# Kernel optimization log

Measured on AMD Instinct MI355X. Metric: run time of the kernel, lower is better.

Reference implementation:

```python
import jax, jax.numpy as jnp
import numpy as np

N_HEAD = 8
N_FEAT = 512
D_K = N_FEAT // N_HEAD


def setup_inputs() -> dict:
    key0 = jax.random.key(0)
    ks = jax.random.split(key0, 12)
    B, C, T, S = 16, 6, 512, 8
    scale = 1.0 / np.sqrt(N_FEAT)
    inp = {
        "query": jax.random.normal(ks[0], (B, C, T, N_FEAT), jnp.float32),
        "key": jax.random.normal(ks[1], (B, S, N_FEAT), jnp.float32),
        "value": jax.random.normal(ks[2], (B, S, N_FEAT), jnp.float32),
        "mask": jnp.ones((B, 1, T, S), jnp.int32),
        "Wq": jax.random.normal(ks[3], (N_FEAT, N_FEAT), jnp.float32) * scale,
        "bq": jax.random.normal(ks[4], (N_FEAT,), jnp.float32) * scale,
        "Wk": jax.random.normal(ks[5], (N_FEAT, N_FEAT), jnp.float32) * scale,
        "bk": jax.random.normal(ks[6], (N_FEAT,), jnp.float32) * scale,
        "Wv": jax.random.normal(ks[7], (N_FEAT, N_FEAT), jnp.float32) * scale,
        "bv": jax.random.normal(ks[8], (N_FEAT,), jnp.float32) * scale,
        "Wo": jax.random.normal(ks[9], (N_FEAT, N_FEAT), jnp.float32) * scale,
        "bo": jax.random.normal(ks[10], (N_FEAT,), jnp.float32) * scale,
    }
    return inp


def reference(query, key, value, mask, Wq, bq, Wk, bk, Wv, bv, Wo, bo):
    B, C, T, F = query.shape
    S = key.shape[-2]
    h, d_k = N_HEAD, D_K
    inv_sqrt_dk = 1.0 / jnp.sqrt(jnp.asarray(d_k, query.dtype))

    # forward_qkv
    qx = jnp.swapaxes(query, 1, 2)                       # (B, T, C, F)
    q = (qx @ Wq.T + bq).reshape(B, T, C, h, d_k)        # (B, T, C, h, d_k)
    k = (key @ Wk.T + bk).reshape(B, S, h, d_k)          # (B, S, h, d_k)
    v = (value @ Wv.T + bv).reshape(B, S, h, d_k)        # (B, S, h, d_k)
    v2 = jnp.swapaxes(q, 2, 3)                           # (B, T, h, C, d_k)
    q1 = q.mean(axis=2)                                  # (B, T, h, d_k)

    # stage 1: mean-pooled query attends over spk_num (masked softmax)
    scores = jnp.einsum('bthd,bshd->bhts', q1, k) * inv_sqrt_dk  # (B, h, T, S)
    m = (mask == 0)                                      # (B, 1, T, S) bool
    scores = jnp.where(m, -jnp.inf, scores)
    attn = jax.nn.softmax(scores, axis=-1)
    attn = jnp.where(m, 0.0, attn)
    phone_ctx = jnp.einsum('bhts,bshd->bthd', attn, v)   # (B, T, h, d_k)

    # stage 2: pooled context attends over channels
    ss = jnp.einsum('bthd,bthcd->bthc', phone_ctx, v2) * inv_sqrt_dk  # (B, T, h, C)
    attn2 = jax.nn.softmax(ss, axis=-1)
    x = jnp.einsum('bthc,bthcd->bthd', attn2, v2).reshape(B, T, h * d_k)
    return x @ Wo.T + bo                                 # (B, T, F)
```

## Files before the change

### kernel.cpp

```cpp
#include <hip/hip_runtime.h>
#include <hip/hip_bf16.h>

#define B_  16
#define C_  6
#define T_  512
#define S_  8

#define AS1 __attribute__((address_space(1)))
#define AS3 __attribute__((address_space(3)))

typedef __attribute__((ext_vector_type(8))) short bf16x8;
typedef __attribute__((ext_vector_type(4))) float f32x4;

__device__ __forceinline__ ushort f2bf(float f) {
    __hip_bfloat16 h = __float2bfloat16(f);
    return *reinterpret_cast<ushort*>(&h);
}
__device__ __forceinline__ float bfu2f(ushort u) {
    uint x = (uint)u << 16;
    union { uint u; float f; } c; c.u = x; return c.f;
}

__global__ void convert_all(const float* __restrict__ Wq, const float* __restrict__ Wo,
                            const float* __restrict__ Wk, const float* __restrict__ Wv,
                            const float* __restrict__ key, const float* __restrict__ value,
                            ushort* __restrict__ dWq, ushort* __restrict__ dWo,
                            ushort* __restrict__ dWk, ushort* __restrict__ dWv,
                            ushort* __restrict__ dkey, ushort* __restrict__ dval) {
    int y = blockIdx.y;
    int i = (blockIdx.x * 256 + threadIdx.x) * 4;
    if (y < 4) {
        const float* s = (y == 0) ? Wq : (y == 1) ? Wo : (y == 2) ? Wk : Wv;
        ushort* d = (y == 0) ? dWq : (y == 1) ? dWo : (y == 2) ? dWk : dWv;
        float4 v = *(const float4*)(s + i);
        ushort4 o;
        o.x = f2bf(v.x); o.y = f2bf(v.y); o.z = f2bf(v.z); o.w = f2bf(v.w);
        *(ushort4*)(d + i) = o;
    } else if (i < 65536) {
        float4 v = *(const float4*)(key + i);
        ushort4 o;
        o.x = f2bf(v.x); o.y = f2bf(v.y); o.z = f2bf(v.z); o.w = f2bf(v.w);
        *(ushort4*)(dkey + i) = o;
        float4 v2 = *(const float4*)(value + i);
        ushort4 o2;
        o2.x = f2bf(v2.x); o2.y = f2bf(v2.y); o2.z = f2bf(v2.z); o2.w = f2bf(v2.w);
        *(ushort4*)(dval + i) = o2;
    }
}

__global__ __launch_bounds__(256, 2) void kvgemm(const ushort* __restrict__ keybf,
                                                 const ushort* __restrict__ valbf,
                                                 const ushort* __restrict__ Wkbf,
                                                 const ushort* __restrict__ Wvbf,
                                                 const float* __restrict__ bk,
                                                 const float* __restrict__ bv,
                                                 float* __restrict__ kout,
                                                 float* __restrict__ vout) {
    __shared__ __align__(16) ushort lds[32768];

    const int kv = blockIdx.x >> 2;
    const int bn = (blockIdx.x & 3) * 128;
    const ushort* Ain = kv ? valbf : keybf;
    const ushort* Wbf = kv ? Wvbf : Wkbf;
    const float* bias = kv ? bv : bk;
    float* out = kv ? vout : kout;

    const int tid  = threadIdx.x;
    const int lane = tid & 63;
    const int wv   = tid >> 6;
    const int wm   = (wv >> 1) * 64;
    const int wn   = (wv & 1) * 64;
    const int ln15 = lane & 15;
    const int ln16 = lane >> 4;

    auto GLDS = [&](const ushort* gbase, int rowbase, ushort* ldsbase, int k0) {
        int rb = wv * 32 + (lane >> 3);
        int c  = lane & 7;
#pragma unroll
        for (int i = 0; i < 4; ++i) {
            int r = rb + i * 8;
            const ushort* src = gbase + (long)(rowbase + r) * 512 + k0 + ((c ^ (r & 7)) << 3);
            ushort* dst = ldsbase + wv * 2048 + i * 512;
            __builtin_amdgcn_global_load_lds((AS1 const void*)src, (AS3 void*)dst, 16, 0, 0);
        }
    };

    ushort* asb0 = lds;
    ushort* asb1 = lds + 8192;
    ushort* wsb[2] = { lds + 16384, lds + 24576 };

    f32x4 acc[4][4] = {};

    auto MFMA_PHASE = [&](ushort* Asb, ushort* Wsb) {
        __builtin_amdgcn_s_setprio(1);
#pragma unroll
        for (int kj = 0; kj < 2; ++kj) {
            bf16x8 af[4], bfv[4];
#pragma unroll
            for (int mi = 0; mi < 4; ++mi) {
                int row = wm + mi * 16 + ln15;
                int ch  = kj * 4 + ln16;
                af[mi] = *(const bf16x8*)&Asb[row * 64 + ((ch ^ (row & 7)) << 3)];
            }
#pragma unroll
            for (int ni = 0; ni < 4; ++ni) {
                int row = wn + ni * 16 + ln15;
                int ch  = kj * 4 + ln16;
                bfv[ni] = *(const bf16x8*)&Wsb[row * 64 + ((ch ^ (row & 7)) << 3)];
            }
#pragma unroll
            for (int mi = 0; mi < 4; ++mi)
#pragma unroll
                for (int ni = 0; ni < 4; ++ni)
                    acc[mi][ni] = __builtin_amdgcn_mfma_f32_16x16x32_bf16(
                        af[mi], bfv[ni], acc[mi][ni], 0, 0, 0);
        }
        __builtin_amdgcn_s_setprio(0);
    };

    GLDS(Ain, 0, asb0, 0);
    GLDS(Wbf, bn, wsb[0], 0);
    asm volatile("s_waitcnt vmcnt(0) lgkmcnt(0)" ::: "memory");
    __builtin_amdgcn_sched_barrier(0);
    __builtin_amdgcn_s_barrier();
    asm volatile("" ::: "memory");
#pragma unroll
    for (int kt = 0; kt < 8; ++kt) {
        ushort* Asb = (kt & 1) ? asb1 : asb0;
        ushort* nAs = (kt & 1) ? asb0 : asb1;
        if (kt < 7) {
            GLDS(Wbf, bn, wsb[(kt + 1) & 1], (kt + 1) * 64);
            GLDS(Ain, 0, nAs, (kt + 1) * 64);
        }
        __builtin_amdgcn_sched_barrier(0);
        MFMA_PHASE(Asb, wsb[kt & 1]);
        asm volatile("s_waitcnt vmcnt(0) lgkmcnt(0)" ::: "memory");
        __builtin_amdgcn_sched_barrier(0);
        __builtin_amdgcn_s_barrier();
        asm volatile("" ::: "memory");
    }

    float bsv[4];
#pragma unroll
    for (int ni = 0; ni < 4; ++ni)
        bsv[ni] = bias[bn + wn + ni * 16 + ln15];

    float* ef = (float*)lds;
#pragma unroll
    for (int half = 0; half < 2; ++half) {
        if (wm == half * 64) {
#pragma unroll
            for (int mi = 0; mi < 4; ++mi)
#pragma unroll
                for (int j = 0; j < 4; ++j) {
                    int lr = mi * 16 + ln16 * 4 + j;
#pragma unroll
                    for (int ni = 0; ni < 4; ++ni) {
                        int col = wn + ni * 16 + ln15;
                        int cs  = col ^ ((lr & 12) << 2);
                        ef[lr * 128 + cs] = acc[mi][ni][j] + bsv[ni];
                    }
                }
        }
        asm volatile("s_waitcnt lgkmcnt(0)" ::: "memory");
        __builtin_amdgcn_sched_barrier(0);
        __builtin_amdgcn_s_barrier();
        asm volatile("" ::: "memory");
#pragma unroll
        for (int i = 0; i < 8; ++i) {
            int idx = i * 1024 + tid * 4;
            int lr = idx >> 7, col = idx & 127;
            int cs = col ^ ((lr & 12) << 2);
            float4 v = *(const float4*)&ef[lr * 128 + cs];
            *(float4*)(out + (long)(half * 64 + lr) * 512 + bn + col) = v;
        }
        if (half == 0) {
            asm volatile("" ::: "memory");
            __builtin_amdgcn_s_barrier();
            asm volatile("" ::: "memory");
        }
    }
}

__global__ __launch_bounds__(512) void qattn(const float* __restrict__ query,
                                             const ushort* __restrict__ Wqbf,
                                             const float* __restrict__ bq,
                                             const float* __restrict__ kproj,
                                             const float* __restrict__ vproj,
                                             const int* __restrict__ mask,
                                             ushort* __restrict__ xout) {
    __shared__ __align__(16) ushort Abf[2][96 * 128];
    __shared__ __align__(16) ushort xstage[16 * 512];
    __shared__ int mlds[256];

    const int b   = blockIdx.x >> 4;
    const int tpb = (blockIdx.x & 15) << 5;
    const int tid = threadIdx.x;
    const int h    = tid >> 6;
    const int lane = tid & 63;
    const int ln15 = lane & 15;
    const int ln16 = lane >> 4;
    const int nb   = h * 64;

    float4 ra[6];
    f32x4 acc[6][4];
    uint4 br[3][4];

    auto LOADQ = [&](int t0, int q) {
#pragma unroll
        for (int i = 0; i < 6; ++i) {
            int idx = i * 2048 + tid * 4;
            int row = idx >> 7;
            int col = idx & 127;
            int c = row >> 4, tt = row & 15;
            ra[i] = *(const float4*)(query + ((long)(b * 6 + c) * 512 + t0 + tt) * 512
                                     + q * 128 + col);
        }
    };
    auto WRITEQ = [&](ushort* buf) {
#pragma unroll
        for (int i = 0; i < 6; ++i) {
            int idx = i * 2048 + tid * 4;
            int row = idx >> 7;
            int col = idx & 127;
            int kc8  = col >> 3;
            int half = (col >> 2) & 1;
            int s = (kc8 & 8) | ((kc8 & 7) ^ (row & 7));
            ushort4 p;
            p.x = f2bf(ra[i].x); p.y = f2bf(ra[i].y);
            p.z = f2bf(ra[i].z); p.w = f2bf(ra[i].w);
            *(ushort4*)((char*)buf + row * 256 + s * 16 + half * 8) = p;
        }
    };
    auto RINGINIT = [&]() {
#pragma unroll
        for (int kb = 0; kb < 3; ++kb)
#pragma unroll
            for (int nf = 0; nf < 4; ++nf)
                br[kb][nf] = *(const uint4*)(Wqbf + (long)(nb + nf * 16 + ln15) * 512
                                             + kb * 32 + ln16 * 8);
    };
#define GEMMQ(BUF, Q)                                                          \
    {                                                                          \
        const ushort* buf_ = (BUF);                                            \
        __builtin_amdgcn_s_setprio(1);                                         \
        _Pragma("unroll")                                                      \
        for (int kb8 = 0; kb8 < 4; ++kb8) {                                    \
            int kb = (Q) * 4 + kb8;                                            \
            bf16x8 af[6];                                                      \
            _Pragma("unroll")                                                  \
            for (int mf = 0; mf < 6; ++mf) {                                   \
                int row = mf * 16 + ln15;                                      \
                int kc8 = kb8 * 4 + ln16;                                      \
                int s = (kc8 & 8) | ((kc8 & 7) ^ (row & 7));                   \
                af[mf] = *(const bf16x8*)((const char*)buf_ + row * 256 + s * 16); \
            }                                                                  \
            _Pragma("unroll")                                                  \
            for (int mf = 0; mf < 6; ++mf)                                     \
                _Pragma("unroll")                                              \
                for (int nf = 0; nf < 4; ++nf)                                 \
                    acc[mf][nf] = __builtin_amdgcn_mfma_f32_16x16x32_bf16(     \
                        af[mf], *(const bf16x8*)&br[kb % 3][nf], acc[mf][nf], 0, 0, 0); \
            if (kb < 13) {                                                     \
                _Pragma("unroll")                                              \
                for (int nf = 0; nf < 4; ++nf)                                 \
                    br[(kb + 3) % 3][nf] = *(const uint4*)(Wqbf +              \
                        (long)(nb + nf * 16 + ln15) * 512 + (kb + 3) * 32 + ln16 * 8); \
            }                                                                  \
        }                                                                      \
        __builtin_amdgcn_s_setprio(0);                                         \
    }

    auto PHASES = [&](int t0, int mloff) {
        {
            float bqv[4];
#pragma unroll
            for (int nf = 0; nf < 4; ++nf) bqv[nf] = bq[nb + nf * 16 + ln15];
#pragma unroll
            for (int mf = 0; mf < 6; ++mf)
#pragma unroll
                for (int nf = 0; nf < 4; ++nf)
#pragma unroll
                    for (int j = 0; j < 4; ++j) acc[mf][nf][j] += bqv[nf];
        }
        f32x4 q1f[4];
#pragma unroll
        for (int nf = 0; nf < 4; ++nf) {
            f32x4 s = acc[0][nf];
#pragma unroll
            for (int c = 1; c < 6; ++c) s += acc[c][nf];
            q1f[nf] = s * (1.0f / 6.0f);
        }
        float sc[4][8];
#pragma unroll
        for (int s = 0; s < 8; ++s) {
            float kv[4];
#pragma unroll
            for (int nf = 0; nf < 4; ++nf)
                kv[nf] = kproj[(long)(b * 8 + s) * 512 + nb + nf * 16 + ln15];
#pragma unroll
            for (int j = 0; j < 4; ++j) {
                float p = q1f[0][j] * kv[0] + q1f[1][j] * kv[1]
                        + q1f[2][j] * kv[2] + q1f[3][j] * kv[3];
                p += __shfl_xor(p, 1); p += __shfl_xor(p, 2);
                p += __shfl_xor(p, 4); p += __shfl_xor(p, 8);
                sc[j][s] = p * 0.125f;
            }
        }
#pragma unroll
        for (int j = 0; j < 4; ++j) {
            int tt = ln16 * 4 + j;
            int mk[8];
            float mx = -1e30f;
#pragma unroll
            for (int s = 0; s < 8; ++s) {
                mk[s] = mlds[mloff + tt * 8 + s];
                if (mk[s] == 0) sc[j][s] = -1e30f;
                mx = fmaxf(mx, sc[j][s]);
            }
            float sum = 0.f;
#pragma unroll
            for (int s = 0; s < 8; ++s) {
                float e = __expf(sc[j][s] - mx);
                sc[j][s] = e;
                sum += e;
            }
            float inv = 1.0f / sum;
#pragma unroll
            for (int s = 0; s < 8; ++s) sc[j][s] = mk[s] ? sc[j][s] * inv : 0.f;
        }
        f32x4 pcf[4] = {};
#pragma unroll
        for (int s = 0; s < 8; ++s) {
            float vv[4];
#pragma unroll
            for (int nf = 0; nf < 4; ++nf)
                vv[nf] = vproj[(long)(b * 8 + s) * 512 + nb + nf * 16 + ln15];
#pragma unroll
            for (int nf = 0; nf < 4; ++nf)
#pragma unroll
                for (int j = 0; j < 4; ++j) pcf[nf][j] += sc[j][s] * vv[nf];
        }
        float a2[4][6];
#pragma unroll
        for (int c = 0; c < 6; ++c)
#pragma unroll
            for (int j = 0; j < 4; ++j) {
                float p = pcf[0][j] * acc[c][0][j] + pcf[1][j] * acc[c][1][j]
                        + pcf[2][j] * acc[c][2][j] + pcf[3][j] * acc[c][3][j];
                p += __shfl_xor(p, 1); p += __shfl_xor(p, 2);
                p += __shfl_xor(p, 4); p += __shfl_xor(p, 8);
                a2[j][c] = p * 0.125f;
            }
#pragma unroll
        for (int j = 0; j < 4; ++j) {
            float mx = -1e30f;
#pragma unroll
            for (int c = 0; c < 6; ++c) mx = fmaxf(mx, a2[j][c]);
            float sum = 0.f;
#pragma unroll
            for (int c = 0; c < 6; ++c) {
                float e = __expf(a2[j][c] - mx);
                a2[j][c] = e;
                sum += e;
            }
            float inv = 1.0f / sum;
#pragma unroll
            for (int c = 0; c < 6; ++c) a2[j][c] *= inv;
        }
#pragma unroll
        for (int nf = 0; nf < 4; ++nf)
#pragma unroll
            for (int j = 0; j < 4; ++j) {
                float x = 0.f;
#pragma unroll
                for (int c = 0; c < 6; ++c) x += a2[j][c] * acc[c][nf][j];
                xstage[(ln16 * 4 + j) * 512 + nb + nf * 16 + ln15] = f2bf(x);
            }
        __syncthreads();
        {
            int idx = tid * 16;
            int row = idx >> 9;
            int off = idx & 511;
            uint4 v0 = *(const uint4*)&xstage[row * 512 + off];
            uint4 v1 = *(const uint4*)&xstage[row * 512 + off + 8];
            ushort* dst = xout + ((long)(b * 512 + t0 + row)) * 512 + off;
            *(uint4*)dst = v0;
            *(uint4*)(dst + 8) = v1;
        }
    };

    const int t0a = tpb;
    const int t0b = tpb + 16;

    if (tid < 256) mlds[tid] = mask[((long)b * 512 + tpb + (tid >> 3)) * 8 + (tid & 7)];

    LOADQ(t0a, 0);
    WRITEQ(Abf[0]);
    __syncthreads();

#pragma unroll
    for (int mf = 0; mf < 6; ++mf)
#pragma unroll
        for (int nf = 0; nf < 4; ++nf) acc[mf][nf] = (f32x4){0.f, 0.f, 0.f, 0.f};
    RINGINIT();

    LOADQ(t0a, 1); __builtin_amdgcn_sched_barrier(0);
    GEMMQ(Abf[0], 0);
    WRITEQ(Abf[1]); __syncthreads();
    LOADQ(t0a, 2); __builtin_amdgcn_sched_barrier(0);
    GEMMQ(Abf[1], 1);
    WRITEQ(Abf[0]); __syncthreads();
    LOADQ(t0a, 3); __builtin_amdgcn_sched_barrier(0);
    GEMMQ(Abf[0], 2);
    WRITEQ(Abf[1]); __syncthreads();
    LOADQ(t0b, 0); __builtin_amdgcn_sched_barrier(0);
    GEMMQ(Abf[1], 3);
    WRITEQ(Abf[0]); __syncthreads();

    LOADQ(t0b, 1); __builtin_amdgcn_sched_barrier(0);
    PHASES(t0a, 0);

    __syncthreads();
    WRITEQ(Abf[1]);
    __syncthreads();

#pragma unroll
    for (int mf = 0; mf < 6; ++mf)
#pragma unroll
        for (int nf = 0; nf < 4; ++nf) acc[mf][nf] = (f32x4){0.f, 0.f, 0.f, 0.f};
    RINGINIT();

    LOADQ(t0b, 2); __builtin_amdgcn_sched_barrier(0);
    GEMMQ(Abf[0], 0);
    WRITEQ(Abf[0]); __syncthreads();
    LOADQ(t0b, 3); __builtin_amdgcn_sched_barrier(0);
    GEMMQ(Abf[1], 1);
    WRITEQ(Abf[1]); __syncthreads();
    GEMMQ(Abf[0], 2);
    __syncthreads();
    GEMMQ(Abf[1], 3);

    PHASES(t0b, 128);
#undef GEMMQ
}

__global__ __launch_bounds__(256, 2)
void gemm_mfma(const void* __restrict__ Ain,
               const ushort* __restrict__ Wbf,
               const float* __restrict__ bias,
               void* __restrict__ out, int mpanels) {
    __shared__ __align__(16) ushort lds[32768];

    const int bid = blockIdx.x;
    const int cpx = (mpanels * 4) >> 3;
    const int swz = (bid & 7) * cpx + (bid >> 3);
    const int bm = (swz >> 2) * 128;
    const int bn = (swz & 3) * 128;

    const int tid  = threadIdx.x;
    const int lane = tid & 63;
    const int wv   = tid >> 6;
    const int wm   = (wv >> 1) * 64;
    const int wn   = (wv & 1) * 64;
    const int ln15 = lane & 15;
    const int ln16 = lane >> 4;

    auto GLDS = [&](const ushort* gbase, int rowbase, ushort* ldsbase, int k0) {
        int rb = wv * 32 + (lane >> 3);
        int c  = lane & 7;
#pragma unroll
        for (int i = 0; i < 4; ++i) {
            int r = rb + i * 8;
            const ushort* src = gbase + (long)(rowbase + r) * 512 + k0 + ((c ^ (r & 7)) << 3);
            ushort* dst = ldsbase + wv * 2048 + i * 512;
            __builtin_amdgcn_global_load_lds((AS1 const void*)src, (AS3 void*)dst, 16, 0, 0);
        }
    };

    ushort* asb0 = lds;
    ushort* asb1 = lds + 8192;
    ushort* wsb[2] = { lds + 16384, lds + 24576 };

    f32x4 acc[4][4] = {};

    auto MFMA_PHASE = [&](ushort* Asb, ushort* Wsb) {
        __builtin_amdgcn_s_setprio(1);
#pragma unroll
        for (int kj = 0; kj < 2; ++kj) {
            bf16x8 af[4], bfv[4];
#pragma unroll
            for (int mi = 0; mi < 4; ++mi) {
                int row = wm + mi * 16 + ln15;
                int ch  = kj * 4 + ln16;
                af[mi] = *(const bf16x8*)&Asb[row * 64 + ((ch ^ (row & 7)) << 3)];
            }
#pragma unroll
            for (int ni = 0; ni < 4; ++ni) {
                int row = wn + ni * 16 + ln15;
                int ch  = kj * 4 + ln16;
                bfv[ni] = *(const bf16x8*)&Wsb[row * 64 + ((ch ^ (row & 7)) << 3)];
            }
#pragma unroll
            for (int mi = 0; mi < 4; ++mi)
#pragma unroll
                for (int ni = 0; ni < 4; ++ni)
                    acc[mi][ni] = __builtin_amdgcn_mfma_f32_16x16x32_bf16(
                        af[mi], bfv[ni], acc[mi][ni], 0, 0, 0);
        }
        __builtin_amdgcn_s_setprio(0);
    };

    GLDS((const ushort*)Ain, bm, asb0, 0);
    GLDS(Wbf, bn, wsb[0], 0);
    asm volatile("s_waitcnt vmcnt(0) lgkmcnt(0)" ::: "memory");
    __builtin_amdgcn_sched_barrier(0);
    __builtin_amdgcn_s_barrier();
    asm volatile("" ::: "memory");
#pragma unroll
    for (int kt = 0; kt < 8; ++kt) {
        ushort* Asb = (kt & 1) ? asb1 : asb0;
        ushort* nAs = (kt & 1) ? asb0 : asb1;
        if (kt < 7) {
            GLDS(Wbf, bn, wsb[(kt + 1) & 1], (kt + 1) * 64);
            GLDS((const ushort*)Ain, bm, nAs, (kt + 1) * 64);
        }
        __builtin_amdgcn_sched_barrier(0);
        MFMA_PHASE(Asb, wsb[kt & 1]);
        asm volatile("s_waitcnt vmcnt(0) lgkmcnt(0)" ::: "memory");
        __builtin_amdgcn_sched_barrier(0);
        __builtin_amdgcn_s_barrier();
        asm volatile("" ::: "memory");
    }

    float bsv[4];
#pragma unroll
    for (int ni = 0; ni < 4; ++ni)
        bsv[ni] = bias[bn + wn + ni * 16 + ln15];

    float* ef = (float*)lds;
#pragma unroll
    for (int half = 0; half < 2; ++half) {
        if (wm == half * 64) {
#pragma unroll
            for (int mi = 0; mi < 4; ++mi)
#pragma unroll
                for (int j = 0; j < 4; ++j) {
                    int lr = mi * 16 + ln16 * 4 + j;
#pragma unroll
                    for (int ni = 0; ni < 4; ++ni) {
                        int col = wn + ni * 16 + ln15;
                        int cs  = col ^ ((lr & 12) << 2);
                        ef[lr * 128 + cs] = acc[mi][ni][j] + bsv[ni];
                    }
                }
        }
        asm volatile("s_waitcnt lgkmcnt(0)" ::: "memory");
        __builtin_amdgcn_sched_barrier(0);
        __builtin_amdgcn_s_barrier();
        asm volatile("" ::: "memory");
#pragma unroll
        for (int i = 0; i < 8; ++i) {
            int idx = i * 1024 + tid * 4;
            int lr = idx >> 7, col = idx & 127;
            int cs = col ^ ((lr & 12) << 2);
            float4 v = *(const float4*)&ef[lr * 128 + cs];
            *(float4*)((float*)out + (long)(bm + half * 64 + lr) * 512 + bn + col) = v;
        }
        if (half == 0) {
            asm volatile("" ::: "memory");
            __builtin_amdgcn_s_barrier();
            asm volatile("" ::: "memory");
        }
    }
}

extern "C" void kernel_launch(void* const* d_in, const int* in_sizes, int n_in,
                              void* d_out, int out_size, void* d_ws, size_t ws_size,
                              hipStream_t stream) {
    const float* query = (const float*)d_in[0];
    const float* key   = (const float*)d_in[1];
    const float* value = (const float*)d_in[2];
    const int*   mask  = (const int*)d_in[3];
    const float* Wq = (const float*)d_in[4];
    const float* bq = (const float*)d_in[5];
    const float* Wk = (const float*)d_in[6];
    const float* bk = (const float*)d_in[7];
    const float* Wv = (const float*)d_in[8];
    const float* bv = (const float*)d_in[9];
    const float* Wo = (const float*)d_in[10];
    const float* bo = (const float*)d_in[11];
    float* out = (float*)d_out;

    char* ws = (char*)d_ws;
    ushort* Wqbf  = (ushort*)(ws + 0);
    ushort* Wobf  = (ushort*)(ws + 524288u);
    ushort* Wkbf  = (ushort*)(ws + 1048576u);
    ushort* Wvbf  = (ushort*)(ws + 1572864u);
    ushort* keybf = (ushort*)(ws + 2097152u);
    ushort* valbf = (ushort*)(ws + 2228224u);
    float*  kproj = (float*)(ws + 2621440u);
    float*  vproj = (float*)(ws + 2883584u);
    ushort* xbf   = (ushort*)(ws + (4u << 20));

    convert_all<<<dim3(256, 5), 256, 0, stream>>>(Wq, Wo, Wk, Wv, key, value,
                                                  Wqbf, Wobf, Wkbf, Wvbf, keybf, valbf);

    kvgemm<<<8, 256, 0, stream>>>(keybf, valbf, Wkbf, Wvbf, bk, bv, kproj, vproj);

    qattn<<<256, 512, 0, stream>>>(query, Wqbf, bq, kproj, vproj, mask, xbf);

    gemm_mfma<<<256, 256, 0, stream>>>(xbf, Wobf, bo, out, 64);

    (void)in_sizes; (void)n_in; (void)out_size; (void)ws_size;
}
```

Measured before the change: 95.08 us.

## Split qattn into one 16-timestep tile per block with two blocks per CU

The qattn kernel now processes a single 16-timestep tile per block instead of two sequential tiles, launching 512 blocks instead of 256. It requests two 512-thread blocks per CU via launch bounds, reuses the A buffer as the output staging area to cut LDS, and uses two register sets to prefetch query chunks. The aim is more concurrency, so one block's GEMM overlaps another's softmax/epilogue and load latency, instead of serial in-block pipelining. The tighter register budget may cause spills, and the Wq fragments are reloaded per block.

New measurement: 83.48 us, median of 2. -12.2%, faster.

```diff
diff --git a/kernel.cpp b/kernel.cpp
--- a/kernel.cpp
+++ b/kernel.cpp
@@ -182,19 +182,18 @@
     }
 }
 
-__global__ __launch_bounds__(512) void qattn(const float* __restrict__ query,
-                                             const ushort* __restrict__ Wqbf,
-                                             const float* __restrict__ bq,
-                                             const float* __restrict__ kproj,
-                                             const float* __restrict__ vproj,
-                                             const int* __restrict__ mask,
-                                             ushort* __restrict__ xout) {
+__global__ __launch_bounds__(512, 2) void qattn(const float* __restrict__ query,
+                                                const ushort* __restrict__ Wqbf,
+                                                const float* __restrict__ bq,
+                                                const float* __restrict__ kproj,
+                                                const float* __restrict__ vproj,
+                                                const int* __restrict__ mask,
+                                                ushort* __restrict__ xout) {
     __shared__ __align__(16) ushort Abf[2][96 * 128];
-    __shared__ __align__(16) ushort xstage[16 * 512];
-    __shared__ int mlds[256];
-
-    const int b   = blockIdx.x >> 4;
-    const int tpb = (blockIdx.x & 15) << 5;
+    __shared__ int mlds[128];
+
+    const int b   = blockIdx.x >> 5;
+    const int t0  = (blockIdx.x & 31) << 4;
     const int tid = threadIdx.x;
     const int h    = tid >> 6;
     const int lane = tid & 63;
@@ -202,11 +201,9 @@
     const int ln16 = lane >> 4;
     const int nb   = h * 64;
 
-    float4 ra[6];
-    f32x4 acc[6][4];
-    uint4 br[3][4];
-
-    auto LOADQ = [&](int t0, int q) {
+    float4 ra0[6], ra1[6];
+
+    auto LOADQ = [&](float4 (&ra)[6], int q) {
 #pragma unroll
         for (int i = 0; i < 6; ++i) {
             int idx = i * 2048 + tid * 4;
@@ -217,7 +214,7 @@
                                      + q * 128 + col);
         }
     };
-    auto WRITEQ = [&](ushort* buf) {
+    auto WRITEQ = [&](float4 (&ra)[6], ushort* buf) {
 #pragma unroll
         for (int i = 0; i < 6; ++i) {
             int idx = i * 2048 + tid * 4;
@@ -232,14 +229,24 @@
             *(ushort4*)((char*)buf + row * 256 + s * 16 + half * 8) = p;
         }
     };
-    auto RINGINIT = [&]() {
-#pragma unroll
-        for (int kb = 0; kb < 3; ++kb)
-#pragma unroll
-            for (int nf = 0; nf < 4; ++nf)
-                br[kb][nf] = *(const uint4*)(Wqbf + (long)(nb + nf * 16 + ln15) * 512
-                                             + kb * 32 + ln16 * 8);
-    };
+
+    if (tid < 128) mlds[tid] = mask[((long)b * 512 + t0 + (tid >> 3)) * 8 + (tid & 7)];
+
+    LOADQ(ra0, 0);
+    WRITEQ(ra0, Abf[0]);
+    LOADQ(ra1, 1);
+    __builtin_amdgcn_sched_barrier(0);
+    __syncthreads();
+
+    f32x4 acc[6][4] = {};
+    uint4 br[3][4];
+#pragma unroll
+    for (int kb = 0; kb < 3; ++kb)
+#pragma unroll
+        for (int nf = 0; nf < 4; ++nf)
+            br[kb][nf] = *(const uint4*)(Wqbf + (long)(nb + nf * 16 + ln15) * 512
+                                         + kb * 32 + ln16 * 8);
+
 #define GEMMQ(BUF, Q)                                                          \
     {                                                                          \
         const ushort* buf_ = (BUF);                                            \
@@ -271,178 +278,146 @@
         __builtin_amdgcn_s_setprio(0);                                         \
     }
 
-    auto PHASES = [&](int t0, int mloff) {
-        {
-            float bqv[4];
-#pragma unroll
-            for (int nf = 0; nf < 4; ++nf) bqv[nf] = bq[nb + nf * 16 + ln15];
-#pragma unroll
-            for (int mf = 0; mf < 6; ++mf)
-#pragma unroll
-                for (int nf = 0; nf < 4; ++nf)
-#pragma unroll
-                    for (int j = 0; j < 4; ++j) acc[mf][nf][j] += bqv[nf];
-        }
-        f32x4 q1f[4];
-#pragma unroll
-        for (int nf = 0; nf < 4; ++nf) {
-            f32x4 s = acc[0][nf];
-#pragma unroll
-            for (int c = 1; c < 6; ++c) s += acc[c][nf];
-            q1f[nf] = s * (1.0f / 6.0f);
-        }
-        float sc[4][8];
+    LOADQ(ra0, 2);
+    __builtin_amdgcn_sched_barrier(0);
+    GEMMQ(Abf[0], 0);
+    WRITEQ(ra1, Abf[1]);
+    __syncthreads();
+
+    LOADQ(ra1, 3);
+    __builtin_amdgcn_sched_barrier(0);
+    GEMMQ(Abf[1], 1);
+    WRITEQ(ra0, Abf[0]);
+    __syncthreads();
+
+    GEMMQ(Abf[0], 2);
+    WRITEQ(ra1, Abf[1]);
+    __syncthreads();
+
+    GEMMQ(Abf[1], 3);
+#undef GEMMQ
+
+    {
+        float bqv[4];
+#pragma unroll
+        for (int nf = 0; nf < 4; ++nf) bqv[nf] = bq[nb + nf * 16 + ln15];
+#pragma unroll
+        for (int mf = 0; mf < 6; ++mf)
+#pragma unroll
+            for (int nf = 0; nf < 4; ++nf)
+#pragma unroll
+                for (int j = 0; j < 4; ++j) acc[mf][nf][j] += bqv[nf];
+    }
+
+    f32x4 q1f[4];
+#pragma unroll
+    for (int nf = 0; nf < 4; ++nf) {
+        f32x4 s = acc[0][nf];
+#pragma unroll
+        for (int c = 1; c < 6; ++c) s += acc[c][nf];
+        q1f[nf] = s * (1.0f / 6.0f);
+    }
+
+    float sc[4][8];
+#pragma unroll
+    for (int s = 0; s < 8; ++s) {
+        float kv[4];
+#pragma unroll
+        for (int nf = 0; nf < 4; ++nf)
+            kv[nf] = kproj[(long)(b * 8 + s) * 512 + nb + nf * 16 + ln15];
+#pragma unroll
+        for (int j = 0; j < 4; ++j) {
+            float p = q1f[0][j] * kv[0] + q1f[1][j] * kv[1]
+                    + q1f[2][j] * kv[2] + q1f[3][j] * kv[3];
+            p += __shfl_xor(p, 1); p += __shfl_xor(p, 2);
+            p += __shfl_xor(p, 4); p += __shfl_xor(p, 8);
+            sc[j][s] = p * 0.125f;
+        }
+    }
+#pragma unroll
+    for (int j = 0; j < 4; ++j) {
+        int tt = ln16 * 4 + j;
+        int mk[8];
+        float mx = -1e30f;
 #pragma unroll
         for (int s = 0; s < 8; ++s) {
-            float kv[4];
-#pragma unroll
-            for (int nf = 0; nf < 4; ++nf)
-                kv[nf] = kproj[(long)(b * 8 + s) * 512 + nb + nf * 16 + ln15];
-#pragma unroll
-            for (int j = 0; j < 4; ++j) {
-                float p = q1f[0][j] * kv[0] + q1f[1][j] * kv[1]
-                        + q1f[2][j] * kv[2] + q1f[3][j] * kv[3];
-                p += __shfl_xor(p, 1); p += __shfl_xor(p, 2);
-                p += __shfl_xor(p, 4); p += __shfl_xor(p, 8);
-                sc[j][s] = p * 0.125f;
-            }
-        }
+            mk[s] = mlds[tt * 8 + s];
+            if (mk[s] == 0) sc[j][s] = -1e30f;
+            mx = fmaxf(mx, sc[j][s]);
+        }
+        float sum = 0.f;
+#pragma unroll
+        for (int s = 0; s < 8; ++s) {
+            float e = __expf(sc[j][s] - mx);
+            sc[j][s] = e;
+            sum += e;
+        }
+        float inv = 1.0f / sum;
+#pragma unroll
+        for (int s = 0; s < 8; ++s) sc[j][s] = mk[s] ? sc[j][s] * inv : 0.f;
+    }
+    f32x4 pcf[4] = {};
+#pragma unroll
+    for (int s = 0; s < 8; ++s) {
+        float vv[4];
+#pragma unroll
+        for (int nf = 0; nf < 4; ++nf)
+            vv[nf] = vproj[(long)(b * 8 + s) * 512 + nb + nf * 16 + ln15];
+#pragma unroll
+        for (int nf = 0; nf < 4; ++nf)
+#pragma unroll
+            for (int j = 0; j < 4; ++j) pcf[nf][j] += sc[j][s] * vv[nf];
+    }
+
+    float a2[4][6];
+#pragma unroll
+    for (int c = 0; c < 6; ++c)
 #pragma unroll
         for (int j = 0; j < 4; ++j) {
-            int tt = ln16 * 4 + j;
-            int mk[8];
-            float mx = -1e30f;
-#pragma unroll
-            for (int s = 0; s < 8; ++s) {
-                mk[s] = mlds[mloff + tt * 8 + s];
-                if (mk[s] == 0) sc[j][s] = -1e30f;
-                mx = fmaxf(mx, sc[j][s]);
-            }
-            float sum = 0.f;
-#pragma unroll
-            for (int s = 0; s < 8; ++s) {
-                float e = __expf(sc[j][s] - mx);
-                sc[j][s] = e;
-                sum += e;
-            }
-            float inv = 1.0f / sum;
-#pragma unroll
-            for (int s = 0; s < 8; ++s) sc[j][s] = mk[s] ? sc[j][s] * inv : 0.f;
-        }
-        f32x4 pcf[4] = {};
-#pragma unroll
-        for (int s = 0; s < 8; ++s) {
-            float vv[4];
-#pragma unroll
-            for (int nf = 0; nf < 4; ++nf)
-                vv[nf] = vproj[(long)(b * 8 + s) * 512 + nb + nf * 16 + ln15];
-#pragma unroll
-            for (int nf = 0; nf < 4; ++nf)
-#pragma unroll
-                for (int j = 0; j < 4; ++j) pcf[nf][j] += sc[j][s] * vv[nf];
-        }
-        float a2[4][6];
-#pragma unroll
-        for (int c = 0; c < 6; ++c)
-#pragma unroll
-            for (int j = 0; j < 4; ++j) {
-                float p = pcf[0][j] * acc[c][0][j] + pcf[1][j] * acc[c][1][j]
-                        + pcf[2][j] * acc[c][2][j] + pcf[3][j] * acc[c][3][j];
-                p += __shfl_xor(p, 1); p += __shfl_xor(p, 2);
-                p += __shfl_xor(p, 4); p += __shfl_xor(p, 8);
-                a2[j][c] = p * 0.125f;
-            }
+            float p = pcf[0][j] * acc[c][0][j] + pcf[1][j] * acc[c][1][j]
+                    + pcf[2][j] * acc[c][2][j] + pcf[3][j] * acc[c][3][j];
+            p += __shfl_xor(p, 1); p += __shfl_xor(p, 2);
+            p += __shfl_xor(p, 4); p += __shfl_xor(p, 8);
+            a2[j][c] = p * 0.125f;
+        }
+#pragma unroll
+    for (int j = 0; j < 4; ++j) {
+        float mx = -1e30f;
+#pragma unroll
+        for (int c = 0; c < 6; ++c) mx = fmaxf(mx, a2[j][c]);
+        float sum = 0.f;
+#pragma unroll
+        for (int c = 0; c < 6; ++c) {
+            float e = __expf(a2[j][c] - mx);
+            a2[j][c] = e;
+            sum += e;
+        }
+        float inv = 1.0f / sum;
+#pragma unroll
+        for (int c = 0; c < 6; ++c) a2[j][c] *= inv;
+    }
+
+    ushort* xstage = Abf[0];
+#pragma unroll
+    for (int nf = 0; nf < 4; ++nf)
 #pragma unroll
         for (int j = 0; j < 4; ++j) {
-            float mx = -1e30f;
-#pragma unroll
-            for (int c = 0; c < 6; ++c) mx = fmaxf(mx, a2[j][c]);
-            float sum = 0.f;
-#pragma unroll
-            for (int c = 0; c < 6; ++c) {
-                float e = __expf(a2[j][c] - mx);
-                a2[j][c] = e;
-                sum += e;
-            }
-            float inv = 1.0f / sum;
-#pragma unroll
-            for (int c = 0; c < 6; ++c) a2[j][c] *= inv;
-        }
-#pragma unroll
-        for (int nf = 0; nf < 4; ++nf)
-#pragma unroll
-            for (int j = 0; j < 4; ++j) {
-                float x = 0.f;
-#pragma unroll
-                for (int c = 0; c < 6; ++c) x += a2[j][c] * acc[c][nf][j];
-                xstage[(ln16 * 4 + j) * 512 + nb + nf * 16 + ln15] = f2bf(x);
-            }
-        __syncthreads();
-        {
-            int idx = tid * 16;
-            int row = idx >> 9;
-            int off = idx & 511;
-            uint4 v0 = *(const uint4*)&xstage[row * 512 + off];
-            uint4 v1 = *(const uint4*)&xstage[row * 512 + off + 8];
-            ushort* dst = xout + ((long)(b * 512 + t0 + row)) * 512 + off;
-            *(uint4*)dst = v0;
-            *(uint4*)(dst + 8) = v1;
-        }
-    };
-
-    const int t0a = tpb;
-    const int t0b = tpb + 16;
-
-    if (tid < 256) mlds[tid] = mask[((long)b * 512 + tpb + (tid >> 3)) * 8 + (tid & 7)];
-
-    LOADQ(t0a, 0);
-    WRITEQ(Abf[0]);
+            float x = 0.f;
+#pragma unroll
+            for (int c = 0; c < 6; ++c) x += a2[j][c] * acc[c][nf][j];
+            xstage[(ln16 * 4 + j) * 512 + nb + nf * 16 + ln15] = f2bf(x);
+        }
     __syncthreads();
-
-#pragma unroll
-    for (int mf = 0; mf < 6; ++mf)
-#pragma unroll
-        for (int nf = 0; nf < 4; ++nf) acc[mf][nf] = (f32x4){0.f, 0.f, 0.f, 0.f};
-    RINGINIT();
-
-    LOADQ(t0a, 1); __builtin_amdgcn_sched_barrier(0);
-    GEMMQ(Abf[0], 0);
-    WRITEQ(Abf[1]); __syncthreads();
-    LOADQ(t0a, 2); __builtin_amdgcn_sched_barrier(0);
-    GEMMQ(Abf[1], 1);
-    WRITEQ(Abf[0]); __syncthreads();
-    LOADQ(t0a, 3); __builtin_amdgcn_sched_barrier(0);
-    GEMMQ(Abf[0], 2);
-    WRITEQ(Abf[1]); __syncthreads();
-    LOADQ(t0b, 0); __builtin_amdgcn_sched_barrier(0);
-    GEMMQ(Abf[1], 3);
-    WRITEQ(Abf[0]); __syncthreads();
-
-    LOADQ(t0b, 1); __builtin_amdgcn_sched_barrier(0);
-    PHASES(t0a, 0);
-
-    __syncthreads();
-    WRITEQ(Abf[1]);
-    __syncthreads();
-
-#pragma unroll
-    for (int mf = 0; mf < 6; ++mf)
-#pragma unroll
-        for (int nf = 0; nf < 4; ++nf) acc[mf][nf] = (f32x4){0.f, 0.f, 0.f, 0.f};
-    RINGINIT();
-
-    LOADQ(t0b, 2); __builtin_amdgcn_sched_barrier(0);
-    GEMMQ(Abf[0], 0);
-    WRITEQ(Abf[0]); __syncthreads();
-    LOADQ(t0b, 3); __builtin_amdgcn_sched_barrier(0);
-    GEMMQ(Abf[1], 1);
-    WRITEQ(Abf[1]); __syncthreads();
-    GEMMQ(Abf[0], 2);
-    __syncthreads();
-    GEMMQ(Abf[1], 3);
-
-    PHASES(t0b, 128);
-#undef GEMMQ
+    {
+        int idx = tid * 16;
+        int row = idx >> 9;
+        int off = idx & 511;
+        uint4 v0 = *(const uint4*)&xstage[row * 512 + off];
+        uint4 v1 = *(const uint4*)&xstage[row * 512 + off + 8];
+        ushort* dst = xout + ((long)(b * 512 + t0 + row)) * 512 + off;
+        *(uint4*)dst = v0;
+        *(uint4*)(dst + 8) = v1;
+    }
 }
 
 __global__ __launch_bounds__(256, 2)
@@ -608,7 +583,7 @@
 
     kvgemm<<<8, 256, 0, stream>>>(keybf, valbf, Wkbf, Wvbf, bk, bv, kproj, vproj);
 
-    qattn<<<256, 512, 0, stream>>>(query, Wqbf, bq, kproj, vproj, mask, xbf);
+    qattn<<<512, 512, 0, stream>>>(query, Wqbf, bq, kproj, vproj, mask, xbf);
 
     gemm_mfma<<<256, 256, 0, stream>>>(xbf, Wobf, bo, out, 64);
 
```

## Double-buffer query register prefetch and reuse A buffer as x staging

Applied to the files above, without the earlier changes.

Adds a second register buffer for query loads so global loads run two k-chunks ahead of the MFMA loop, and rearranges the LOADQ/WRITEQ schedule to match. Drops the separate xstage LDS array by aliasing it onto Abf[0], which cuts LDS per block. Also sets launch bounds to allow two 512-thread blocks per CU. The extra 24 registers of prefetch state add register pressure under the tighter occupancy bound, which could cause spills. Aliasing the staging area onto Abf also relies on correct barrier placement around PHASES.

New measurement: 100.2 us. 1.05x slower.

```diff
diff --git a/kernel.cpp b/kernel.cpp
--- a/kernel.cpp
+++ b/kernel.cpp
@@ -182,31 +182,30 @@
     }
 }
 
-__global__ __launch_bounds__(512) void qattn(const float* __restrict__ query,
-                                             const ushort* __restrict__ Wqbf,
-                                             const float* __restrict__ bq,
-                                             const float* __restrict__ kproj,
-                                             const float* __restrict__ vproj,
-                                             const int* __restrict__ mask,
-                                             ushort* __restrict__ xout) {
+__global__ __launch_bounds__(512, 2) void qattn(const float* __restrict__ query,
+                                                const ushort* __restrict__ Wqbf,
+                                                const float* __restrict__ bq,
+                                                const float* __restrict__ kproj,
+                                                const float* __restrict__ vproj,
+                                                const int* __restrict__ mask,
+                                                ushort* __restrict__ xout) {
     __shared__ __align__(16) ushort Abf[2][96 * 128];
-    __shared__ __align__(16) ushort xstage[16 * 512];
     __shared__ int mlds[256];
 
-    const int b   = blockIdx.x >> 4;
-    const int tpb = (blockIdx.x & 15) << 5;
-    const int tid = threadIdx.x;
+    const int b    = blockIdx.x >> 4;
+    const int tpb  = (blockIdx.x & 15) << 5;
+    const int tid  = threadIdx.x;
     const int h    = tid >> 6;
     const int lane = tid & 63;
     const int ln15 = lane & 15;
     const int ln16 = lane >> 4;
     const int nb   = h * 64;
 
-    float4 ra[6];
+    float4 ra0[6], ra1[6];
     f32x4 acc[6][4];
     uint4 br[3][4];
 
-    auto LOADQ = [&](int t0, int q) {
+    auto LOADQ = [&](float4 (&ra)[6], int t0, int q) {
 #pragma unroll
         for (int i = 0; i < 6; ++i) {
             int idx = i * 2048 + tid * 4;
@@ -217,7 +216,7 @@
                                      + q * 128 + col);
         }
     };
-    auto WRITEQ = [&](ushort* buf) {
+    auto WRITEQ = [&](float4 (&ra)[6], ushort* buf) {
 #pragma unroll
         for (int i = 0; i < 6; ++i) {
             int idx = i * 2048 + tid * 4;
@@ -240,6 +239,7 @@
                 br[kb][nf] = *(const uint4*)(Wqbf + (long)(nb + nf * 16 + ln15) * 512
                                              + kb * 32 + ln16 * 8);
     };
+
 #define GEMMQ(BUF, Q)                                                          \
     {                                                                          \
         const ushort* buf_ = (BUF);                                            \
@@ -368,6 +368,7 @@
 #pragma unroll
             for (int c = 0; c < 6; ++c) a2[j][c] *= inv;
         }
+        ushort* xstage = Abf[0];
 #pragma unroll
         for (int nf = 0; nf < 4; ++nf)
 #pragma unroll
@@ -395,8 +396,10 @@
 
     if (tid < 256) mlds[tid] = mask[((long)b * 512 + tpb + (tid >> 3)) * 8 + (tid & 7)];
 
-    LOADQ(t0a, 0);
-    WRITEQ(Abf[0]);
+    LOADQ(ra0, t0a, 0);
+    WRITEQ(ra0, Abf[0]);
+    LOADQ(ra1, t0a, 1);
+    __builtin_amdgcn_sched_barrier(0);
     __syncthreads();
 
 #pragma unroll
@@ -405,24 +408,33 @@
         for (int nf = 0; nf < 4; ++nf) acc[mf][nf] = (f32x4){0.f, 0.f, 0.f, 0.f};
     RINGINIT();
 
-    LOADQ(t0a, 1); __builtin_amdgcn_sched_barrier(0);
+    LOADQ(ra0, t0a, 2);
+    __builtin_amdgcn_sched_barrier(0);
     GEMMQ(Abf[0], 0);
-    WRITEQ(Abf[1]); __syncthreads();
-    LOADQ(t0a, 2); __builtin_amdgcn_sched_barrier(0);
+    WRITEQ(ra1, Abf[1]);
+    __syncthreads();
+
+    LOADQ(ra1, t0a, 3);
+    __builtin_amdgcn_sched_barrier(0);
     GEMMQ(Abf[1], 1);
-    WRITEQ(Abf[0]); __syncthreads();
-    LOADQ(t0a, 3); __builtin_amdgcn_sched_barrier(0);
+    WRITEQ(ra0, Abf[0]);
+    __syncthreads();
+
     GEMMQ(Abf[0], 2);
-    WRITEQ(Abf[1]); __syncthreads();
-    LOADQ(t0b, 0); __builtin_amdgcn_sched_barrier(0);
+    WRITEQ(ra1, Abf[1]);
+    __syncthreads();
+
     GEMMQ(Abf[1], 3);
-    WRITEQ(Abf[0]); __syncthreads();
-
-    LOADQ(t0b, 1); __builtin_amdgcn_sched_barrier(0);
+
+    LOADQ(ra0, t0b, 0);
+    __builtin_amdgcn_sched_barrier(0);
+
     PHASES(t0a, 0);
-
-    __syncthreads();
-    WRITEQ(Abf[1]);
+    __syncthreads();
+
+    WRITEQ(ra0, Abf[0]);
+    LOADQ(ra1, t0b, 1);
+    __builtin_amdgcn_sched_barrier(0);
     __syncthreads();
 
 #pragma unroll
@@ -431,14 +443,22 @@
         for (int nf = 0; nf < 4; ++nf) acc[mf][nf] = (f32x4){0.f, 0.f, 0.f, 0.f};
     RINGINIT();
 
-    LOADQ(t0b, 2); __builtin_amdgcn_sched_barrier(0);
+    LOADQ(ra0, t0b, 2);
+    __builtin_amdgcn_sched_barrier(0);
     GEMMQ(Abf[0], 0);
-    WRITEQ(Abf[0]); __syncthreads();
-    LOADQ(t0b, 3); __builtin_amdgcn_sched_barrier(0);
+    WRITEQ(ra1, Abf[1]);
+    __syncthreads();
+
+    LOADQ(ra1, t0b, 3);
+    __builtin_amdgcn_sched_barrier(0);
     GEMMQ(Abf[1], 1);
-    WRITEQ(Abf[1]); __syncthreads();
+    WRITEQ(ra0, Abf[0]);
+    __syncthreads();
+
     GEMMQ(Abf[0], 2);
-    __syncthreads();
+    WRITEQ(ra1, Abf[1]);
+    __syncthreads();
+
     GEMMQ(Abf[1], 3);
 
     PHASES(t0b, 128);
```
